# Kernel optimization log

Measured on AMD Instinct MI355X. Metric: run time of the kernel, lower is better.

## Reference

```python
import jax, jax.numpy as jnp
import numpy as np

N = 50000   # nodes
E = 500000  # edges
G = 64      # graphs in batch
H = 2       # attention heads
D = 64      # hidden per head (hid)
F_IN = 4    # num_features
C = 5       # num_classes
NEG_SLOPE = 0.2


def setup_inputs() -> dict:
    key = jax.random.key(0)
    ks = jax.random.split(key, 24)
    inp = {
        'x': jax.random.normal(ks[0], (N, F_IN), jnp.float32),
        'edge_index': jax.random.randint(ks[1], (2, E), 0, N, dtype=jnp.int64),
        'batch': jnp.sort(jax.random.randint(ks[2], (N,), 0, G, dtype=jnp.int64)),
    }
    ins = [F_IN, H * D, H * D, H * D]
    ki = 3
    for l, fin in enumerate(ins, 1):
        s = 1.0 / np.sqrt(fin)
        inp[f'W{l}'] = s * jax.random.normal(ks[ki], (fin, H * D), jnp.float32); ki += 1
        inp[f'asrc{l}'] = 0.1 * jax.random.normal(ks[ki], (H, D), jnp.float32); ki += 1
        inp[f'adst{l}'] = 0.1 * jax.random.normal(ks[ki], (H, D), jnp.float32); ki += 1
        inp[f'b{l}'] = 0.01 * jax.random.normal(ks[ki], (H * D,), jnp.float32); ki += 1
    inp['lin_w'] = (1.0 / np.sqrt(H * D)) * jax.random.normal(ks[ki], (H * D, C), jnp.float32); ki += 1
    inp['lin_b'] = jnp.zeros((C,), jnp.float32)
    return inp


def gat_conv(x, src, dst, W, a_src, a_dst, b):
    # x: [N, Fin] -> h: [N, H, D]
    h = (x @ W).reshape(-1, H, D)
    alpha_src = jnp.sum(h * a_src, axis=-1)  # [N, H]
    alpha_dst = jnp.sum(h * a_dst, axis=-1)  # [N, H]
    e = jax.nn.leaky_relu(alpha_src[src] + alpha_dst[dst], NEG_SLOPE)  # [E, H]
    # segment softmax over incoming edges of each dst node
    e_max = jax.ops.segment_max(e, dst, num_segments=N)  # [N, H]
    e_exp = jnp.exp(e - e_max[dst])
    denom = jax.ops.segment_sum(e_exp, dst, num_segments=N)
    alpha = e_exp / (denom[dst] + 1e-16)  # [E, H]
    msg = h[src] * alpha[:, :, None]  # [E, H, D]
    out = jax.ops.segment_sum(msg, dst, num_segments=N)  # [N, H, D]
    return out.reshape(-1, H * D) + b


def reference(x, edge_index, batch,
              W1, asrc1, adst1, b1,
              W2, asrc2, adst2, b2,
              W3, asrc3, adst3, b3,
              W4, asrc4, adst4, b4,
              lin_w, lin_b):
    src, dst = edge_index[0], edge_index[1]
    h = jax.nn.relu(gat_conv(x, src, dst, W1, asrc1, adst1, b1))
    h = jax.nn.relu(gat_conv(h, src, dst, W2, asrc2, adst2, b2))
    h = jax.nn.relu(gat_conv(h, src, dst, W3, asrc3, adst3, b3))
    h = jax.nn.relu(gat_conv(h, src, dst, W4, asrc4, adst4, b4))
    # global mean pool over graphs
    sums = jax.ops.segment_sum(h, batch, num_segments=G)  # [G, 128]
    counts = jax.ops.segment_sum(jnp.ones((h.shape[0],), h.dtype), batch, num_segments=G)
    pooled = sums / jnp.maximum(counts, 1.0)[:, None]
    return jax.nn.sigmoid(pooled @ lin_w + lin_b)  # [G, C]
```

## Files before the change

kernel.cpp:

```cpp
#include <hip/hip_runtime.h>
#include <math.h>

#define NHEAD 2
#define NDIM  64
#define HD    128
#define NGRAPH 64
#define NCLS  5
#define NEG_SLOPE 0.2f

typedef __attribute__((ext_vector_type(8))) short bf16x8;
typedef __attribute__((ext_vector_type(4))) float f32x4;

static __device__ __forceinline__ unsigned short f2bf(float f) {
    unsigned int u = __float_as_uint(f);
    u = (u + 0x7fff + ((u >> 16) & 1)) >> 16;
    return (unsigned short)u;
}
static __device__ __forceinline__ float bf2f(unsigned short b) {
    return __uint_as_float((unsigned int)b << 16);
}


__global__ void k_deg(const int* __restrict__ dst, int* __restrict__ deg, int E) {
    int i = blockIdx.x * blockDim.x + threadIdx.x;
    if (i < E) atomicAdd(&deg[dst[i]], 1);
}

__global__ __launch_bounds__(256) void k_scan_local(const int* __restrict__ deg,
                                                    int* __restrict__ ptr,
                                                    int* __restrict__ bsum, int n) {
    __shared__ int wsum[4];
    const int tid = threadIdx.x, lane = tid & 63, wid = tid >> 6;
    const int base = blockIdx.x * 2048 + tid * 8;
    int v[8];
    #pragma unroll
    for (int k = 0; k < 8; ++k) {
        int i = base + k;
        v[k] = (i < n) ? deg[i] : 0;
    }
    #pragma unroll
    for (int k = 1; k < 8; ++k) v[k] += v[k - 1];
    int x = v[7];
    #pragma unroll
    for (int off = 1; off < 64; off <<= 1) {
        int t = __shfl_up(x, off, 64);
        if (lane >= off) x += t;
    }
    if (lane == 63) wsum[wid] = x;
    __syncthreads();
    int woff = 0;
    #pragma unroll
    for (int k = 0; k < 4; ++k) woff += (k < wid) ? wsum[k] : 0;
    int texcl = woff + x - v[7];
    #pragma unroll
    for (int k = 0; k < 8; ++k) {
        int i = base + k;
        if (i < n) ptr[i + 1] = texcl + v[k];
    }
    if (tid == 255) bsum[blockIdx.x] = woff + x;
    if (blockIdx.x == 0 && tid == 0) ptr[0] = 0;
}

__global__ void k_scan_bsum(int* __restrict__ bsum, int B) {
    int lane = threadIdx.x;
    int carry = 0;
    for (int base = 0; base < B; base += 64) {
        int i = base + lane;
        int v = (i < B) ? bsum[i] : 0;
        int x = v;
        #pragma unroll
        for (int off = 1; off < 64; off <<= 1) {
            int t = __shfl_up(x, off, 64);
            if (lane >= off) x += t;
        }
        if (i < B) bsum[i] = carry + x - v;
        carry += __shfl(x, 63, 64);
    }
}

__global__ __launch_bounds__(256) void k_scan_add(int* __restrict__ ptr,
                                                  const int* __restrict__ bsum, int n) {
    int off = bsum[blockIdx.x];
    if (off == 0) return;
    const int base = blockIdx.x * 2048 + threadIdx.x * 8;
    #pragma unroll
    for (int k = 0; k < 8; ++k) {
        int i = base + k;
        if (i < n) ptr[i + 1] += off;
    }
}

__global__ void k_scatter(const int* __restrict__ src, const int* __restrict__ dst,
                          const int* __restrict__ ptr, int* __restrict__ fill,
                          int* __restrict__ csr, int E) {
    int i = blockIdx.x * blockDim.x + threadIdx.x;
    if (i < E) {
        int d = dst[i];
        int pos = atomicAdd(&fill[d], 1);
        csr[ptr[d] + pos] = src[i];
    }
}


__global__ void k_prepw(const float* __restrict__ W2, const float* __restrict__ W3,
                        const float* __restrict__ W4, unsigned short* __restrict__ Wt) {
    int idx = blockIdx.x * blockDim.x + threadIdx.x;
    if (idx >= 3 * HD * HD) return;
    int l = idx / (HD * HD), rem = idx % (HD * HD);
    int n = rem >> 7, k = rem & 127;
    const float* W = (l == 0) ? W2 : (l == 1) ? W3 : W4;
    Wt[idx] = f2bf(W[k * HD + n]);
}


__global__ void k_gemm1(const float* __restrict__ x, const float* __restrict__ W,
                        unsigned short* __restrict__ out, int N) {
    int idx = blockIdx.x * blockDim.x + threadIdx.x;
    if (idx >= N * HD) return;
    int node = idx >> 7, col = idx & 127;
    float4 xv = *(const float4*)&x[node * 4];
    float v = xv.x * W[col] + xv.y * W[128 + col] + xv.z * W[256 + col] + xv.w * W[384 + col];
    out[idx] = f2bf(v);
}

#define LDA 136
__global__ __launch_bounds__(256) void k_gemm_mfma(const unsigned short* __restrict__ A,
                                                   const unsigned short* __restrict__ Wt,
                                                   const float* __restrict__ asrc,
                                                   const float* __restrict__ adst,
                                                   unsigned short* __restrict__ out,
                                                   float* __restrict__ oas,
                                                   float* __restrict__ oad, int N) {
    __shared__ unsigned short As[128 * LDA];
    __shared__ unsigned short Ws[128 * LDA];
    const int tid = threadIdx.x;
    const int nbase = blockIdx.x * 128;
    const int lane = tid & 63, w = tid >> 6;
    const int l15 = lane & 15, quad = lane >> 4;
    const int koff = quad * 8;

    for (int c = tid; c < 2048; c += 256) {
        int row = c >> 4, k8 = (c & 15) << 3;
        int g = nbase + row;
        uint4 v = make_uint4(0, 0, 0, 0);
        if (g < N) v = *(const uint4*)&A[(size_t)g * HD + k8];
        *(uint4*)&As[row * LDA + k8] = v;
    }
    for (int c = tid; c < 2048; c += 256) {
        int row = c >> 4, k8 = (c & 15) << 3;
        *(uint4*)&Ws[row * LDA + k8] = *(const uint4*)&Wt[row * HD + k8];
    }
    float av[8], dv[8];
    #pragma unroll
    for (int c = 0; c < 8; ++c) {
        av[c] = asrc[c * 16 + l15];
        dv[c] = adst[c * 16 + l15];
    }
    __syncthreads();

    f32x4 acc0[8], acc1[8];
    #pragma unroll
    for (int c = 0; c < 8; ++c) { acc0[c] = (f32x4)(0.f); acc1[c] = (f32x4)(0.f); }

    const int r0 = w * 32 + l15;
    #pragma unroll
    for (int ks = 0; ks < 4; ++ks) {
        bf16x8 a0 = *(const bf16x8*)&As[r0 * LDA + ks * 32 + koff];
        bf16x8 a1 = *(const bf16x8*)&As[(r0 + 16) * LDA + ks * 32 + koff];
        #pragma unroll
        for (int c = 0; c < 8; ++c) {
            bf16x8 b = *(const bf16x8*)&Ws[(c * 16 + l15) * LDA + ks * 32 + koff];
            acc0[c] = __builtin_amdgcn_mfma_f32_16x16x32_bf16(a0, b, acc0[c], 0, 0, 0);
            acc1[c] = __builtin_amdgcn_mfma_f32_16x16x32_bf16(a1, b, acc1[c], 0, 0, 0);
        }
    }

    #pragma unroll
    for (int i = 0; i < 2; ++i) {
        int rowb = nbase + w * 32 + i * 16 + quad * 4;
        #pragma unroll
        for (int c = 0; c < 8; ++c) {
            f32x4 v = i ? acc1[c] : acc0[c];
            int col = c * 16 + l15;
            #pragma unroll
            for (int r = 0; r < 4; ++r) {
                int row = rowb + r;
                if (row < N) out[(size_t)row * HD + col] = f2bf(v[r]);
            }
        }
        #pragma unroll
        for (int r = 0; r < 4; ++r) {
            float ps0 = 0.f, ps1 = 0.f, pd0 = 0.f, pd1 = 0.f;
            #pragma unroll
            for (int c = 0; c < 4; ++c) {
                float hv = i ? acc1[c][r] : acc0[c][r];
                ps0 += hv * av[c]; pd0 += hv * dv[c];
            }
            #pragma unroll
            for (int c = 4; c < 8; ++c) {
                float hv = i ? acc1[c][r] : acc0[c][r];
                ps1 += hv * av[c]; pd1 += hv * dv[c];
            }
            #pragma unroll
            for (int off = 1; off < 16; off <<= 1) {
                ps0 += __shfl_xor(ps0, off);
                ps1 += __shfl_xor(ps1, off);
                pd0 += __shfl_xor(pd0, off);
                pd1 += __shfl_xor(pd1, off);
            }
            int row = rowb + r;
            if (l15 == 0 && row < N) {
                *(float2*)&oas[row * 2] = make_float2(ps0, ps1);
                *(float2*)&oad[row * 2] = make_float2(pd0, pd1);
            }
        }
    }
}

__global__ void k_alpha(const unsigned short* __restrict__ h, const float* __restrict__ asrc,
                        const float* __restrict__ adst, float* __restrict__ oas,
                        float* __restrict__ oad, int N) {
    int n = (blockIdx.x * blockDim.x + threadIdx.x) >> 6;
    int lane = threadIdx.x & 63;
    if (n >= N) return;
    ushort2 uv = *(const ushort2*)&h[(size_t)n * HD + lane * 2];
    float vx = bf2f(uv.x), vy = bf2f(uv.y);
    float2 av = *(const float2*)&asrc[lane * 2];
    float2 dv = *(const float2*)&adst[lane * 2];
    float s = vx * av.x + vy * av.y;
    float t = vx * dv.x + vy * dv.y;
    #pragma unroll
    for (int off = 16; off > 0; off >>= 1) {
        s += __shfl_xor(s, off);
        t += __shfl_xor(t, off);
    }
    if ((lane & 31) == 0) {
        int head = lane >> 5;
        oas[n * 2 + head] = s;
        oad[n * 2 + head] = t;
    }
}

__global__ void k_agg(const unsigned short* __restrict__ h, const float* __restrict__ oas,
                      const float* __restrict__ oad, const int* __restrict__ ptr,
                      const int* __restrict__ csr, const float* __restrict__ bias,
                      unsigned short* __restrict__ out, int N) {
    int n = (blockIdx.x * blockDim.x + threadIdx.x) >> 6;
    int lane = threadIdx.x & 63;
    if (n >= N) return;
    int beg = ptr[n], end = ptr[n + 1];
    if (beg == end) {
        float2 b2 = *(const float2*)&bias[lane * 2];
        unsigned int packed = (unsigned int)f2bf(fmaxf(b2.x, 0.f)) |
                              ((unsigned int)f2bf(fmaxf(b2.y, 0.f)) << 16);
        *(unsigned int*)&out[(size_t)n * HD + lane * 2] = packed;
        return;
    }
    const int quad = lane >> 4, sub = lane & 15;
    const int hsel = sub >> 3;
    float2 adn = *(const float2*)&oad[n * 2];
    float m0 = -INFINITY, m1 = -INFINITY, l0 = 0.f, l1 = 0.f;
    float acc[8];
    #pragma unroll
    for (int k = 0; k < 8; ++k) acc[k] = 0.f;

    for (int cbeg = beg; cbeg < end; cbeg += 64) {
        int cnt = min(64, end - cbeg);
        int s = 0;
        float e0 = -INFINITY, e1 = -INFINITY;
        if (lane < cnt) {
            s = csr[cbeg + lane];
            float2 as = *(const float2*)&oas[s * 2];
            e0 = as.x + adn.x; e0 = (e0 >= 0.f) ? e0 : NEG_SLOPE * e0;
            e1 = as.y + adn.y; e1 = (e1 >= 0.f) ? e1 : NEG_SLOPE * e1;
        }
        float c0 = e0, c1 = e1;
        #pragma unroll
        for (int off = 32; off > 0; off >>= 1) {
            c0 = fmaxf(c0, __shfl_xor(c0, off));
            c1 = fmaxf(c1, __shfl_xor(c1, off));
        }
        float nm0 = fmaxf(m0, c0), nm1 = fmaxf(m1, c1);
        float sc0 = __expf(m0 - nm0), sc1 = __expf(m1 - nm1);
        float p0 = (lane < cnt) ? __expf(e0 - nm0) : 0.f;
        float p1 = (lane < cnt) ? __expf(e1 - nm1) : 0.f;
        float s0 = p0, s1 = p1;
        #pragma unroll
        for (int off = 32; off > 0; off >>= 1) {
            s0 += __shfl_xor(s0, off);
            s1 += __shfl_xor(s1, off);
        }
        l0 = l0 * sc0 + s0;
        l1 = l1 * sc1 + s1;
        m0 = nm0; m1 = nm1;
        float scl = hsel ? sc1 : sc0;
        #pragma unroll
        for (int k = 0; k < 8; ++k) acc[k] *= scl;

        for (int j = 0; j < cnt; j += 4) {
            int jq = j + quad;
            int sj = __shfl(s, jq);
            float pa = __shfl(p0, jq);
            float pb = __shfl(p1, jq);
            float pj = hsel ? pb : pa;
            uint4 hv = *(const uint4*)&h[(size_t)sj * HD + sub * 8];
            #pragma unroll
            for (int k = 0; k < 4; ++k) {
                unsigned int u = (&hv.x)[k];
                acc[2 * k]     += pj * __uint_as_float(u << 16);
                acc[2 * k + 1] += pj * __uint_as_float(u & 0xffff0000u);
            }
        }
    }
    #pragma unroll
    for (int k = 0; k < 8; ++k) {
        acc[k] += __shfl_xor(acc[k], 16);
        acc[k] += __shfl_xor(acc[k], 32);
    }
    if (quad == 0) {
        float lsel = hsel ? l1 : l0;
        float inv = 1.f / (lsel + 1e-16f);
        float4 ba = *(const float4*)&bias[sub * 8];
        float4 bb = *(const float4*)&bias[sub * 8 + 4];
        float o[8];
        o[0] = fmaxf(acc[0] * inv + ba.x, 0.f);
        o[1] = fmaxf(acc[1] * inv + ba.y, 0.f);
        o[2] = fmaxf(acc[2] * inv + ba.z, 0.f);
        o[3] = fmaxf(acc[3] * inv + ba.w, 0.f);
        o[4] = fmaxf(acc[4] * inv + bb.x, 0.f);
        o[5] = fmaxf(acc[5] * inv + bb.y, 0.f);
        o[6] = fmaxf(acc[6] * inv + bb.z, 0.f);
        o[7] = fmaxf(acc[7] * inv + bb.w, 0.f);
        uint4 pk;
        pk.x = (unsigned int)f2bf(o[0]) | ((unsigned int)f2bf(o[1]) << 16);
        pk.y = (unsigned int)f2bf(o[2]) | ((unsigned int)f2bf(o[3]) << 16);
        pk.z = (unsigned int)f2bf(o[4]) | ((unsigned int)f2bf(o[5]) << 16);
        pk.w = (unsigned int)f2bf(o[6]) | ((unsigned int)f2bf(o[7]) << 16);
        *(uint4*)&out[(size_t)n * HD + sub * 8] = pk;
    }
}

__global__ void k_pool(const unsigned short* __restrict__ feat, const int* __restrict__ batch,
                       float* __restrict__ pooled, int* __restrict__ gcount, int N) {
    int col = threadIdx.x;
    int n0 = blockIdx.x * 128;
    int n1 = min(n0 + 128, N);
    float acc = 0.f;
    int curg = -1, runlen = 0;
    for (int n = n0; n < n1; ++n) {
        int g = batch[n];
        if (g != curg) {
            if (curg >= 0) {
                atomicAdd(&pooled[curg * HD + col], acc);
                if (col == 0) atomicAdd(&gcount[curg], runlen);
            }
            acc = 0.f; runlen = 0;
            curg = g;
        }
        acc += bf2f(feat[(size_t)n * HD + col]);
        runlen++;
    }
    if (curg >= 0) {
        atomicAdd(&pooled[curg * HD + col], acc);
        if (col == 0) atomicAdd(&gcount[curg], runlen);
    }
}

__global__ void k_final(const float* __restrict__ pooled, const int* __restrict__ gcount,
                        const float* __restrict__ lw, const float* __restrict__ lb,
                        float* __restrict__ out) {
    int tid = threadIdx.x;
    if (tid >= NGRAPH * NCLS) return;
    int g = tid / NCLS, c = tid % NCLS;
    float cnt = fmaxf((float)gcount[g], 1.f);
    const float* p = pooled + g * HD;
    float sum = 0.f;
    for (int k = 0; k < HD; ++k)
        sum += p[k] * lw[k * NCLS + c];
    float z = lb[c] + sum / cnt;
    out[tid] = 1.f / (1.f + __expf(-z));
}


static inline size_t al256(size_t x) { return (x + 255) & ~(size_t)255; }

extern "C" void kernel_launch(void* const* d_in, const int* in_sizes, int n_in,
                              void* d_out, int out_size, void* d_ws, size_t ws_size,
                              hipStream_t stream) {
    const int N = in_sizes[0] / 4;
    const int E = in_sizes[1] / 2;

    const float* x     = (const float*)d_in[0];
    const int*   esrc  = (const int*)d_in[1];
    const int*   edst  = esrc + E;
    const int*   batch = (const int*)d_in[2];
    const float* Wl[4]  = {(const float*)d_in[3],  (const float*)d_in[7],
                           (const float*)d_in[11], (const float*)d_in[15]};
    const float* asr[4] = {(const float*)d_in[4],  (const float*)d_in[8],
                           (const float*)d_in[12], (const float*)d_in[16]};
    const float* ads[4] = {(const float*)d_in[5],  (const float*)d_in[9],
                           (const float*)d_in[13], (const float*)d_in[17]};
    const float* bs[4]  = {(const float*)d_in[6],  (const float*)d_in[10],
                           (const float*)d_in[14], (const float*)d_in[18]};
    const float* lin_w = (const float*)d_in[19];
    const float* lin_b = (const float*)d_in[20];
    float* out = (float*)d_out;

    char* w = (char*)d_ws;
    size_t off = 0;
    auto alloc = [&](size_t bytes) -> void* {
        void* p = w + off;
        off = al256(off + bytes);
        return p;
    };
    int*   deg    = (int*)alloc((size_t)N * 4);
    int*   fill   = (int*)alloc((size_t)N * 4);
    int*   gcount = (int*)alloc((size_t)NGRAPH * 4);
    float* pooled = (float*)alloc((size_t)NGRAPH * HD * 4);
    size_t zbytes = off;
    int*   ptr    = (int*)alloc((size_t)(N + 1) * 4);
    int*   bsum   = (int*)alloc((size_t)1024 * 4);
    int*   csr    = (int*)alloc((size_t)E * 4);
    unsigned short* hbuf = (unsigned short*)alloc((size_t)N * HD * 2);
    unsigned short* feat = (unsigned short*)alloc((size_t)N * HD * 2);
    unsigned short* Wt   = (unsigned short*)alloc((size_t)3 * HD * HD * 2);
    float* a_src  = (float*)alloc((size_t)N * 2 * 4);
    float* a_dst  = (float*)alloc((size_t)N * 2 * 4);
    (void)ws_size; (void)n_in; (void)out_size;

    hipMemsetAsync(d_ws, 0, zbytes, stream);

    k_prepw<<<(3 * HD * HD + 255) / 256, 256, 0, stream>>>(Wl[1], Wl[2], Wl[3], Wt);
    k_deg<<<(E + 255) / 256, 256, 0, stream>>>(edst, deg, E);
    const int SB = (N + 2047) / 2048;
    k_scan_local<<<SB, 256, 0, stream>>>(deg, ptr, bsum, N);
    k_scan_bsum<<<1, 64, 0, stream>>>(bsum, SB);
    k_scan_add<<<SB, 256, 0, stream>>>(ptr, bsum, N);
    k_scatter<<<(E + 255) / 256, 256, 0, stream>>>(esrc, edst, ptr, fill, csr, E);

    const int node_wave_blocks = (N + 3) / 4;

    for (int layer = 0; layer < 4; ++layer) {
        if (layer == 0) {
            k_gemm1<<<(N * HD + 255) / 256, 256, 0, stream>>>(x, Wl[0], hbuf, N);
            k_alpha<<<node_wave_blocks, 256, 0, stream>>>(hbuf, asr[0], ads[0], a_src, a_dst, N);
        } else {
            k_gemm_mfma<<<(N + 127) / 128, 256, 0, stream>>>(
                feat, Wt + (size_t)(layer - 1) * HD * HD,
                asr[layer], ads[layer], hbuf, a_src, a_dst, N);
        }
        k_agg<<<node_wave_blocks, 256, 0, stream>>>(hbuf, a_src, a_dst, ptr, csr, bs[layer], feat, N);
    }

    k_pool<<<(N + 127) / 128, 128, 0, stream>>>(feat, batch, pooled, gcount, N);
    k_final<<<1, 320, 0, stream>>>(pooled, gcount, lin_w, lin_b, out);
}
```

Before: 404.2 us.

## Fuse layer-1 GEMM with alpha and software-pipeline neighbor feature loads in aggregation

Merges the first-layer projection and the attention-logit kernel into one kernel, so the hidden features are computed and reduced in registers without a write-then-reread and one launch disappears. In the aggregation kernel, the gathers of neighbor feature rows are issued before the softmax max/sum reductions and then run through a two-deep register pipeline, so gather latency overlaps the shuffle reductions and the accumulation. The cost is more live registers per thread, which may lower occupancy.

```diff
diff --git a/kernel.cpp b/kernel.cpp
--- a/kernel.cpp
+++ b/kernel.cpp
@@ -112,15 +112,39 @@
     Wt[idx] = f2bf(W[k * HD + n]);
 }
 
-
-__global__ void k_gemm1(const float* __restrict__ x, const float* __restrict__ W,
-                        unsigned short* __restrict__ out, int N) {
-    int idx = blockIdx.x * blockDim.x + threadIdx.x;
-    if (idx >= N * HD) return;
-    int node = idx >> 7, col = idx & 127;
-    float4 xv = *(const float4*)&x[node * 4];
-    float v = xv.x * W[col] + xv.y * W[128 + col] + xv.z * W[256 + col] + xv.w * W[384 + col];
-    out[idx] = f2bf(v);
+__global__ void k_gemm1_alpha(const float* __restrict__ x, const float* __restrict__ W,
+                              const float* __restrict__ asrc, const float* __restrict__ adst,
+                              unsigned short* __restrict__ out, float* __restrict__ oas,
+                              float* __restrict__ oad, int N) {
+    int n = (blockIdx.x * blockDim.x + threadIdx.x) >> 6;
+    int lane = threadIdx.x & 63;
+    if (n >= N) return;
+    float4 xv = *(const float4*)&x[n * 4];
+    int c0 = lane * 2;
+    float2 w0 = *(const float2*)&W[c0];
+    float2 w1 = *(const float2*)&W[128 + c0];
+    float2 w2 = *(const float2*)&W[256 + c0];
+    float2 w3 = *(const float2*)&W[384 + c0];
+    float v0 = xv.x * w0.x + xv.y * w1.x + xv.z * w2.x + xv.w * w3.x;
+    float v1 = xv.x * w0.y + xv.y * w1.y + xv.z * w2.y + xv.w * w3.y;
+    unsigned short b0 = f2bf(v0), b1 = f2bf(v1);
+    unsigned int packed = (unsigned int)b0 | ((unsigned int)b1 << 16);
+    *(unsigned int*)&out[(size_t)n * HD + c0] = packed;
+    float vx = bf2f(b0), vy = bf2f(b1);
+    float2 av = *(const float2*)&asrc[c0];
+    float2 dv = *(const float2*)&adst[c0];
+    float s = vx * av.x + vy * av.y;
+    float t = vx * dv.x + vy * dv.y;
+    #pragma unroll
+    for (int off = 16; off > 0; off >>= 1) {
+        s += __shfl_xor(s, off);
+        t += __shfl_xor(t, off);
+    }
+    if ((lane & 31) == 0) {
+        int head = lane >> 5;
+        oas[n * 2 + head] = s;
+        oad[n * 2 + head] = t;
+    }
 }
 
 #define LDA 136
@@ -217,30 +241,6 @@
     }
 }
 
-__global__ void k_alpha(const unsigned short* __restrict__ h, const float* __restrict__ asrc,
-                        const float* __restrict__ adst, float* __restrict__ oas,
-                        float* __restrict__ oad, int N) {
-    int n = (blockIdx.x * blockDim.x + threadIdx.x) >> 6;
-    int lane = threadIdx.x & 63;
-    if (n >= N) return;
-    ushort2 uv = *(const ushort2*)&h[(size_t)n * HD + lane * 2];
-    float vx = bf2f(uv.x), vy = bf2f(uv.y);
-    float2 av = *(const float2*)&asrc[lane * 2];
-    float2 dv = *(const float2*)&adst[lane * 2];
-    float s = vx * av.x + vy * av.y;
-    float t = vx * dv.x + vy * dv.y;
-    #pragma unroll
-    for (int off = 16; off > 0; off >>= 1) {
-        s += __shfl_xor(s, off);
-        t += __shfl_xor(t, off);
-    }
-    if ((lane & 31) == 0) {
-        int head = lane >> 5;
-        oas[n * 2 + head] = s;
-        oad[n * 2 + head] = t;
-    }
-}
-
 __global__ void k_agg(const unsigned short* __restrict__ h, const float* __restrict__ oas,
                       const float* __restrict__ oad, const int* __restrict__ ptr,
                       const int* __restrict__ csr, const float* __restrict__ bias,
@@ -264,12 +264,31 @@
     #pragma unroll
     for (int k = 0; k < 8; ++k) acc[k] = 0.f;
 
+    auto accum = [&](uint4 hv, float pj) {
+        #pragma unroll
+        for (int k = 0; k < 4; ++k) {
+            unsigned int u = (&hv.x)[k];
+            acc[2 * k]     += pj * __uint_as_float(u << 16);
+            acc[2 * k + 1] += pj * __uint_as_float(u & 0xffff0000u);
+        }
+    };
+
     for (int cbeg = beg; cbeg < end; cbeg += 64) {
         int cnt = min(64, end - cbeg);
+        int ng = (cnt + 3) >> 2;
         int s = 0;
+        if (lane < cnt) s = csr[cbeg + lane];
+
+        int sjA = __shfl(s, quad);
+        uint4 hA = *(const uint4*)&h[(size_t)sjA * HD + sub * 8];
+        uint4 hB = make_uint4(0, 0, 0, 0);
+        if (ng > 1) {
+            int sjB = __shfl(s, 4 + quad);
+            hB = *(const uint4*)&h[(size_t)sjB * HD + sub * 8];
+        }
+
         float e0 = -INFINITY, e1 = -INFINITY;
         if (lane < cnt) {
-            s = csr[cbeg + lane];
             float2 as = *(const float2*)&oas[s * 2];
             e0 = as.x + adn.x; e0 = (e0 >= 0.f) ? e0 : NEG_SLOPE * e0;
             e1 = as.y + adn.y; e1 = (e1 >= 0.f) ? e1 : NEG_SLOPE * e1;
@@ -297,20 +316,25 @@
         #pragma unroll
         for (int k = 0; k < 8; ++k) acc[k] *= scl;
 
-        for (int j = 0; j < cnt; j += 4) {
-            int jq = j + quad;
-            int sj = __shfl(s, jq);
-            float pa = __shfl(p0, jq);
-            float pb = __shfl(p1, jq);
-            float pj = hsel ? pb : pa;
-            uint4 hv = *(const uint4*)&h[(size_t)sj * HD + sub * 8];
-            #pragma unroll
-            for (int k = 0; k < 4; ++k) {
-                unsigned int u = (&hv.x)[k];
-                acc[2 * k]     += pj * __uint_as_float(u << 16);
-                acc[2 * k + 1] += pj * __uint_as_float(u & 0xffff0000u);
-            }
-        }
+        float paA = __shfl(p0, quad),     pbA = __shfl(p1, quad);
+        float pA  = hsel ? pbA : paA;
+        float pB = 0.f;
+        if (ng > 1) {
+            float paB = __shfl(p0, 4 + quad), pbB = __shfl(p1, 4 + quad);
+            pB = hsel ? pbB : paB;
+        }
+        for (int g = 2; g < ng; ++g) {
+            int jq = g * 4 + quad;
+            int sjC = __shfl(s, jq);
+            float paC = __shfl(p0, jq), pbC = __shfl(p1, jq);
+            float pC  = hsel ? pbC : paC;
+            uint4 hC = *(const uint4*)&h[(size_t)sjC * HD + sub * 8];
+            accum(hA, pA);
+            hA = hB; pA = pB;
+            hB = hC; pB = pC;
+        }
+        accum(hA, pA);
+        if (ng > 1) accum(hB, pB);
     }
     #pragma unroll
     for (int k = 0; k < 8; ++k) {
@@ -442,8 +466,8 @@
 
     for (int layer = 0; layer < 4; ++layer) {
         if (layer == 0) {
-            k_gemm1<<<(N * HD + 255) / 256, 256, 0, stream>>>(x, Wl[0], hbuf, N);
-            k_alpha<<<node_wave_blocks, 256, 0, stream>>>(hbuf, asr[0], ads[0], a_src, a_dst, N);
+            k_gemm1_alpha<<<node_wave_blocks, 256, 0, stream>>>(
+                x, Wl[0], asr[0], ads[0], hbuf, a_src, a_dst, N);
         } else {
             k_gemm_mfma<<<(N + 127) / 128, 256, 0, stream>>>(
                 feat, Wt + (size_t)(layer - 1) * HD * HD,
```

New measurement: 399.1 us. Within noise of the previous version (-1.3%).
